# Optimization experiments

Measured on AMD Instinct MI355X. Metric: run time of the kernel, lower is better.

## Reference

```python
import jax, jax.numpy as jnp
import numpy as np

jax.config.update("jax_enable_x64", True)  # 64-bit hashes for collision-free WL signatures

N_NODES = 100_000
N_FEATURES = 64
N_EDGES = 6_400_000
NUM_ITERATIONS = 3
STEP = 1


def setup_inputs() -> dict:
    key = jax.random.key(0)
    kx, ke = jax.random.split(key)
    x = jax.random.normal(kx, (N_NODES, N_FEATURES), dtype=jnp.float32)  # one-hot-ish label scores
    edge_index = jax.random.randint(ke, (2, N_EDGES), 0, N_NODES, dtype=jnp.int64)
    return {"x": x, "edge_index": edge_index}


def _splitmix64(z):
    # High-quality 64-bit mixer (uint64, wraps mod 2^64).
    z = z + jnp.uint64(0x9E3779B97F4A7C15)
    z = (z ^ (z >> jnp.uint64(30))) * jnp.uint64(0xBF58476D1CE4E5B9)
    z = (z ^ (z >> jnp.uint64(27))) * jnp.uint64(0x94D049BB133111EB)
    return z ^ (z >> jnp.uint64(31))


def _wl_conv(colors, src, dst, offset):
    """One WL refinement: hash (own color, multiset of neighbor colors), then
    relabel signatures by first-occurrence order (matches PyG WLConv's dict
    insertion order), continuing the global color counter `offset` (matches the
    persistent hashmap across iterations)."""
    n = colors.shape[0]
    h = _splitmix64(colors.astype(jnp.uint64) + jnp.uint64(1))
    # multiset of neighbor colors -> order-invariant sum of neighbor hashes
    nb_sum = jnp.zeros(n, dtype=jnp.uint64).at[dst].add(h[src])  # [N]
    sig = _splitmix64(h * jnp.uint64(0x100000001B3) + nb_sum)    # [N] signatures
    # first-occurrence relabeling (stable, deterministic)
    _, inv = jnp.unique(sig, size=n, fill_value=jnp.uint64(0), return_inverse=True)
    idx = jnp.arange(n, dtype=jnp.int64)
    first_idx = jax.ops.segment_min(idx, inv, num_segments=n)  # empty segments -> int64 max
    order = jnp.argsort(first_idx)                              # real uniques come first
    ranks = jnp.zeros(n, dtype=jnp.int64).at[order].set(idx)
    new_colors = offset + ranks[inv]
    num_new = jnp.sum(first_idx < n).astype(jnp.int64)
    return new_colors, offset + num_new


def reference(x, edge_index):
    src, dst = edge_index[0], edge_index[1]
    colors = jnp.argmax(x, axis=1).astype(jnp.int64)  # [N]
    feats = [colors]
    offset = jnp.int64(0)
    for _ in range(NUM_ITERATIONS):
        for _ in range(STEP):
            colors, offset = _wl_conv(colors, src, dst, offset)
        feats.append(colors)
    return jnp.stack(feats, axis=-1)  # [N, NUM_ITERATIONS+1], int64
```

## Files before the change

### kernel.cpp

```cpp
#include <hip/hip_runtime.h>

typedef unsigned long long u64;
typedef unsigned int u32;
typedef unsigned char u8;
typedef int  v4i __attribute__((ext_vector_type(4)));
typedef unsigned int v4u __attribute__((ext_vector_type(4)));

#define TBL_BITS 18
#define TBL_SIZE (1u << TBL_BITS)
#define TBL_MASK (TBL_SIZE - 1u)
#define EMPTY_KEY 0xFFFFFFFFFFFFFFFFull

#define BK_BITS 9
#define BK_SZ   512
#define MAXNB   256
#define PBLK    2048
#define LDSE    3200
#define NSUB    8
#define GSTR    16

__device__ __forceinline__ u64 splitmix64(u64 z) {
    z = z + 0x9E3779B97F4A7C15ull;
    z = (z ^ (z >> 30)) * 0xBF58476D1CE4E5B9ull;
    z = (z ^ (z >> 27)) * 0x94D049BB133111EBull;
    return z ^ (z >> 31);
}

__device__ __forceinline__ v4i nt_load4(const int* p) {
    return __builtin_nontemporal_load((const v4i*)p);
}
__device__ __forceinline__ v4u nt_loadu4(const u32* p) {
    return __builtin_nontemporal_load((const v4u*)p);
}

__global__ __launch_bounds__(256) void partition_argmax(const float* __restrict__ x,
                                                        const int* __restrict__ src,
                                                        const int* __restrict__ dst,
                                                        u32* __restrict__ gcur,
                                                        u32* __restrict__ packed,
                                                        u64* __restrict__ h,
                                                        int* __restrict__ out,
                                                        int n, int mI4, int nbuck, int cap, int per) {
    int t = threadIdx.x, b = blockIdx.x;
    {
        int wv = (b * 256 + t) >> 6, lane = t & 63;
        const int WPG = (PBLK * 256) >> 6;
        for (int row = wv; row < n; row += WPG) {
            float v = x[(size_t)row * 64 + lane];
            int idx = lane;
            #pragma unroll
            for (int off = 32; off >= 1; off >>= 1) {
                float ov = __shfl_xor(v, off);
                int   oi = __shfl_xor(idx, off);
                if (ov > v || (ov == v && oi < idx)) { v = ov; idx = oi; }
            }
            if (lane == 0) {
                h[row] = splitmix64((u64)idx + 1ull);
                out[(size_t)row * 4 + 0] = idx;
            }
        }
    }
    __shared__ u32 pk[LDSE];
    __shared__ u32 spk[LDSE];
    __shared__ u8  bd[LDSE];
    __shared__ u8  sbd[LDSE];
    __shared__ u32 hist[256], adjB[256], cur[256];
    __shared__ u32 wsum[4];
    hist[t] = 0u;
    __syncthreads();
    int i0 = b * per;
    int i1 = i0 + per; if (i1 > mI4) i1 = mI4;
    int nI = i1 - i0; if (nI < 0) nI = 0;
    int nE = nI * 4;
    for (int i = t; i < nI; i += 256) {
        v4i dv = nt_load4(dst + 4 * (size_t)(i0 + i));
        v4i sv = nt_load4(src + 4 * (size_t)(i0 + i));
        u32 d, s, bid;
        d = (u32)dv.x; s = (u32)sv.x; bid = d >> BK_BITS;
        pk[4*i+0] = (s << BK_BITS) | (d & (BK_SZ-1u)); bd[4*i+0] = (u8)bid; atomicAdd(&hist[bid], 1u);
        d = (u32)dv.y; s = (u32)sv.y; bid = d >> BK_BITS;
        pk[4*i+1] = (s << BK_BITS) | (d & (BK_SZ-1u)); bd[4*i+1] = (u8)bid; atomicAdd(&hist[bid], 1u);
        d = (u32)dv.z; s = (u32)sv.z; bid = d >> BK_BITS;
        pk[4*i+2] = (s << BK_BITS) | (d & (BK_SZ-1u)); bd[4*i+2] = (u8)bid; atomicAdd(&hist[bid], 1u);
        d = (u32)dv.w; s = (u32)sv.w; bid = d >> BK_BITS;
        pk[4*i+3] = (s << BK_BITS) | (d & (BK_SZ-1u)); bd[4*i+3] = (u8)bid; atomicAdd(&hist[bid], 1u);
    }
    __syncthreads();
    u32 v = hist[t];
    int lane = t & 63, w = t >> 6;
    int x2 = (int)v;
    #pragma unroll
    for (int o = 1; o < 64; o <<= 1) {
        int y = __shfl_up(x2, o);
        if (lane >= o) x2 += y;
    }
    if (lane == 63) wsum[w] = (u32)x2;
    __syncthreads();
    u32 woff = 0;
    for (int ww = 0; ww < w; ++ww) woff += wsum[ww];
    u32 excl = woff + (u32)x2 - v;
    cur[t] = excl;
    if (t < nbuck && v > 0u) {
        u32 bpos = atomicAdd(&gcur[t * GSTR], v);
        if (bpos > (u32)cap - v) bpos = (u32)cap - v;
        adjB[t] = (u32)t * (u32)cap + bpos - excl;
    }
    __syncthreads();
    for (int i = t; i < nE; i += 256) {
        u32 bb = (u32)bd[i];
        u32 p = atomicAdd(&cur[bb], 1u);
        spk[p] = pk[i];
        sbd[p] = (u8)bb;
    }
    __syncthreads();
    for (int p = t; p < nE; p += 256) {
        packed[adjB[sbd[p]] + (u32)p] = spk[p];
    }
}

__global__ __launch_bounds__(256) void nb_kernel(const u32* __restrict__ packed,
                                                 const u32* __restrict__ gcur,
                                                 const u64* __restrict__ h,
                                                 u64* __restrict__ nb8, size_t nstride,
                                                 u64* __restrict__ keys,
                                                 u32* __restrict__ vals, int nbuck, int cap) {
    int b = blockIdx.x, t = threadIdx.x;
    if (b >= nbuck * NSUB) {
        int base = (b - nbuck * NSUB) * 1024;
        for (int k = t; k < 1024; k += 256) { keys[base + k] = EMPTY_KEY; vals[base + k] = 0xFFFFFFFFu; }
        return;
    }
    int bucket = b >> 3, sub = b & 7;
    __shared__ u64 acc[BK_SZ];
    acc[t] = 0ull; acc[t + 256] = 0ull;
    __syncthreads();
    u32 lo = (u32)bucket * (u32)cap;
    u32 len = gcur[bucket * GSTR];
    u32 q0 = ((len * (u32)sub) >> 3) & ~3u;
    u32 q1 = (sub == 7) ? len : (((len * (u32)(sub + 1)) >> 3) & ~3u);
    u32 nv4 = (q1 - q0) >> 2;
    const u32* pbase = packed + lo + q0;
    for (u32 i = (u32)t; i < nv4; i += 256) {
        v4u vv = nt_loadu4(pbase + 4 * (size_t)i);
        atomicAdd(&acc[vv.x & (BK_SZ - 1u)], h[vv.x >> BK_BITS]);
        atomicAdd(&acc[vv.y & (BK_SZ - 1u)], h[vv.y >> BK_BITS]);
        atomicAdd(&acc[vv.z & (BK_SZ - 1u)], h[vv.z >> BK_BITS]);
        atomicAdd(&acc[vv.w & (BK_SZ - 1u)], h[vv.w >> BK_BITS]);
    }
    for (u32 e = q0 + nv4 * 4 + (u32)t; e < q1; e += 256) {
        u32 vv = packed[lo + e];
        atomicAdd(&acc[vv & (BK_SZ - 1u)], h[vv >> BK_BITS]);
    }
    __syncthreads();
    u64* dstp = nb8 + (size_t)sub * nstride + ((size_t)bucket << BK_BITS);
    dstp[t] = acc[t];
    dstp[t + 256] = acc[t + 256];
}

__global__ void sig_kernel8(const u64* __restrict__ h, const u64* __restrict__ nb8,
                            size_t nstride, u32* __restrict__ slotarr,
                            u64* __restrict__ keys, u32* __restrict__ vals, int n) {
    int i = blockIdx.x * blockDim.x + threadIdx.x;
    if (i >= n) return;
    u64 nbv = 0;
    #pragma unroll
    for (int s = 0; s < NSUB; ++s) nbv += nb8[(size_t)s * nstride + i];
    u64 sg = splitmix64(h[i] * 0x100000001B3ull + nbv);
    u32 slot = (u32)sg & TBL_MASK;
    while (true) {
        u64 k = keys[slot];
        if (k == sg) break;
        if (k == EMPTY_KEY) {
            u64 prev = atomicCAS(&keys[slot], (u64)EMPTY_KEY, sg);
            if (prev == EMPTY_KEY || prev == sg) break;
        }
        slot = (slot + 1u) & TBL_MASK;
    }
    atomicMin(&vals[slot], (u32)i);
    slotarr[i] = slot;
}

__global__ void sig_kernel1(const u64* __restrict__ h, const u64* __restrict__ nb,
                            u32* __restrict__ slotarr, u64* __restrict__ keys,
                            u32* __restrict__ vals, int n) {
    int i = blockIdx.x * blockDim.x + threadIdx.x;
    if (i >= n) return;
    u64 sg = splitmix64(h[i] * 0x100000001B3ull + nb[i]);
    u32 slot = (u32)sg & TBL_MASK;
    while (true) {
        u64 k = keys[slot];
        if (k == sg) break;
        if (k == EMPTY_KEY) {
            u64 prev = atomicCAS(&keys[slot], (u64)EMPTY_KEY, sg);
            if (prev == EMPTY_KEY || prev == sg) break;
        }
        slot = (slot + 1u) & TBL_MASK;
    }
    atomicMin(&vals[slot], (u32)i);
    slotarr[i] = slot;
}

__global__ void count_rank(const u32* __restrict__ slotarr, const u32* __restrict__ vals,
                           u32* __restrict__ f, u32* __restrict__ lrank,
                           u32* __restrict__ partials, int n) {
    int b = blockIdx.x, t = threadIdx.x;
    int i = b * 256 + t;
    u32 isf = 0, fi = 0;
    if (i < n) {
        fi = vals[slotarr[i]];
        f[i] = fi;
        isf = (fi == (u32)i) ? 1u : 0u;
    }
    __shared__ u32 wsum[4];
    u32 lane = t & 63, wv = (u32)t >> 6;
    int x = (int)isf;
    #pragma unroll
    for (int o = 1; o < 64; o <<= 1) {
        int y = __shfl_up(x, o);
        if (lane >= (u32)o) x += y;
    }
    if (lane == 63) wsum[wv] = (u32)x;
    __syncthreads();
    u32 woff = 0;
    for (u32 w = 0; w < wv; ++w) woff += wsum[w];
    if (i < n) lrank[i] = woff + (u32)x - isf;
    if (t == 255) partials[b] = woff + (u32)x;
}

__global__ __launch_bounds__(512) void relabel_fused(const u32* __restrict__ f,
                                                     const u32* __restrict__ lrank,
                                                     const u32* __restrict__ partials,
                                                     u32* __restrict__ offsets, int iter,
                                                     u64* __restrict__ h, int* __restrict__ out,
                                                     int n, int npb) {
    __shared__ u32 pp[512];
    __shared__ u32 ws[8];
    int t = threadIdx.x;
    u32 v = (t < npb) ? partials[t] : 0u;
    int lane = t & 63, w = t >> 6;
    int x = (int)v;
    #pragma unroll
    for (int o = 1; o < 64; o <<= 1) {
        int y = __shfl_up(x, o);
        if (lane >= o) x += y;
    }
    if (lane == 63) ws[w] = (u32)x;
    __syncthreads();
    u32 woff = 0;
    for (int ww = 0; ww < w; ++ww) woff += ws[ww];
    u32 incl = woff + (u32)x;
    pp[t] = incl - v;
    if (blockIdx.x == 0 && t == 511) offsets[iter + 1] = offsets[iter] + incl;
    __syncthreads();
    int i = blockIdx.x * 512 + t;
    if (i >= n) return;
    u32 j = f[i];
    u32 c = offsets[iter] + pp[j >> 8] + lrank[j];
    h[i] = splitmix64((u64)c + 1ull);
    out[(size_t)i * 4 + (iter + 1)] = (int)c;
}


__global__ void argmax_kernel(const float* __restrict__ x, u64* __restrict__ h,
                              int* __restrict__ out, u32* __restrict__ offsets, int n) {
    if (blockIdx.x == 0 && threadIdx.x == 0) offsets[0] = 0u;
    int wave = (int)((blockIdx.x * (u32)blockDim.x + threadIdx.x) >> 6);
    int lane = threadIdx.x & 63;
    if (wave >= n) return;
    float v = x[(size_t)wave * 64 + lane];
    int idx = lane;
    #pragma unroll
    for (int off = 32; off >= 1; off >>= 1) {
        float ov = __shfl_xor(v, off);
        int   oi = __shfl_xor(idx, off);
        if (ov > v || (ov == v && oi < idx)) { v = ov; idx = oi; }
    }
    if (lane == 0) {
        h[wave] = splitmix64((u64)idx + 1ull);
        out[(size_t)wave * 4 + 0] = idx;
    }
}

__global__ void init_iter_kernel(u64* __restrict__ keys, u32* __restrict__ vals,
                                 u64* __restrict__ nb, int n) {
    int i = blockIdx.x * blockDim.x + threadIdx.x;
    if (i < (int)TBL_SIZE) { keys[i] = EMPTY_KEY; vals[i] = 0xFFFFFFFFu; }
    if (i < n) nb[i] = 0ull;
}

__global__ void edge_kernel(const int* __restrict__ src, const int* __restrict__ dst,
                            const u64* __restrict__ h, u64* __restrict__ nb, int m) {
    int stride = gridDim.x * blockDim.x;
    for (int e = blockIdx.x * blockDim.x + threadIdx.x; e < m; e += stride) {
        atomicAdd(&nb[(u32)dst[e]], h[(u32)src[e]]);
    }
}

extern "C" void kernel_launch(void* const* d_in, const int* in_sizes, int n_in,
                              void* d_out, int out_size, void* d_ws, size_t ws_size,
                              hipStream_t stream) {
    const float* x = (const float*)d_in[0];
    const int* ei = (const int*)d_in[1];
    int n = in_sizes[0] / 64;
    int m = in_sizes[1] / 2;
    const int* src = ei;
    const int* dst = ei + m;
    int* out = (int*)d_out;

    const int NPB = (n + 255) / 256;
    const int NRB = (n + 511) / 512;
    const int nbuck = (n + BK_SZ - 1) >> BK_BITS;
    const size_t nstride = (size_t)nbuck << BK_BITS;
    const int mI4 = m >> 2;
    const int per = (mI4 + PBLK - 1) / PBLK;
    const int cap = (int)((((size_t)m / (size_t)(nbuck > 0 ? nbuck : 1)) * 9 / 8 + 2048 + 255) & ~(size_t)255);

    auto align = [](size_t v) { return (v + 255) & ~(size_t)255; };
    const size_t meta_bytes = ((size_t)(MAXNB * GSTR) + 16) * 4;
    size_t sz_meta   = align(meta_bytes);
    size_t sz_packed = align((size_t)nbuck * (size_t)cap * 4);
    size_t sz_h      = align((size_t)n * 8);
    size_t sz_nbp    = align(nstride * 8 * NSUB);
    size_t sz_tblk   = align((size_t)TBL_SIZE * 8);
    size_t sz_tblv   = align((size_t)TBL_SIZE * 4);
    size_t sz_n4     = align((size_t)n * 4);
    size_t sz_small  = align((size_t)512 * 4);
    size_t need_fast = sz_meta + sz_packed + sz_h + sz_nbp + sz_tblk + sz_tblv
                     + 3 * sz_n4 + sz_small + 256;

    char* p = (char*)d_ws;
    bool fast = (ws_size >= need_fast) && (nbuck <= MAXNB) && ((m & 3) == 0)
              && (NPB <= 512) && (per * 4 <= LDSE) && (n >= 256);
    if (fast) {
        u32* meta    = (u32*)p; p += sz_meta;
        u32* gcur    = meta;
        u32* offsets = meta + MAXNB * GSTR;
        u32* packed  = (u32*)p; p += sz_packed;
        u64* h       = (u64*)p; p += sz_h;
        u64* nbp     = (u64*)p; p += sz_nbp;
        u64* keys    = (u64*)p; p += sz_tblk;
        u32* vals    = (u32*)p; p += sz_tblv;
        u32* slotarr = (u32*)p; p += sz_n4;
        u32* f       = (u32*)p; p += sz_n4;
        u32* lrank   = (u32*)p; p += sz_n4;
        u32* partials= (u32*)p;

        hipMemsetAsync(d_ws, 0, meta_bytes, stream);
        partition_argmax<<<PBLK, 256, 0, stream>>>(x, src, dst, gcur, packed, h, out,
                                                   n, mI4, nbuck, cap, per);
        for (int it = 0; it < 3; ++it) {
            nb_kernel    <<<nbuck * NSUB + 256, 256, 0, stream>>>(packed, gcur, h,
                                                                  nbp, nstride, keys, vals, nbuck, cap);
            sig_kernel8  <<<NPB, 256, 0, stream>>>(h, nbp, nstride, slotarr, keys, vals, n);
            count_rank   <<<NPB, 256, 0, stream>>>(slotarr, vals, f, lrank, partials, n);
            relabel_fused<<<NRB, 512, 0, stream>>>(f, lrank, partials, offsets, it, h, out, n, NPB);
        }
    } else {
        u64* h       = (u64*)p; p += sz_h;
        u64* nb      = (u64*)p; p += sz_h;
        u64* keys    = (u64*)p; p += sz_tblk;
        u32* vals    = (u32*)p; p += sz_tblv;
        u32* slotarr = (u32*)p; p += sz_n4;
        u32* f       = (u32*)p; p += sz_n4;
        u32* lrank   = (u32*)p; p += sz_n4;
        u32* partials= (u32*)p; p += sz_small;
        u32* offsets = (u32*)p;

        argmax_kernel<<<(n + 3) / 4, 256, 0, stream>>>(x, h, out, offsets, n);
        for (int it = 0; it < 3; ++it) {
            init_iter_kernel<<<(TBL_SIZE + 255) / 256, 256, 0, stream>>>(keys, vals, nb, n);
            edge_kernel  <<<4096, 256, 0, stream>>>(src, dst, h, nb, m);
            sig_kernel1  <<<NPB, 256, 0, stream>>>(h, nb, slotarr, keys, vals, n);
            count_rank   <<<NPB, 256, 0, stream>>>(slotarr, vals, f, lrank, partials, n);
            relabel_fused<<<NRB, 512, 0, stream>>>(f, lrank, partials, offsets, it, h, out, n, NPB);
        }
    }
}
```

Measured before the change: 266.1 us.

## Split argmax from partition, halve nb sub-splits, separate partial scan from relabel

Three changes are bundled. The argmax is moved out of the fused partition kernel into its own one-wave-per-row launch. The per-bucket neighbor accumulation now uses 4 sub-blocks instead of 8, so the signature kernel sums four partial arrays instead of eight. The fused relabel kernel, where every block redundantly scanned the block partials, is replaced by a single-block scan kernel plus a 256-thread relabel kernel. This cuts redundant scan work and partial-sum traffic, but adds kernel launches per iteration and gives less parallelism in nb_kernel.

```diff
diff --git a/kernel.cpp b/kernel.cpp
--- a/kernel.cpp
+++ b/kernel.cpp
@@ -16,7 +16,7 @@
 #define MAXNB   256
 #define PBLK    2048
 #define LDSE    3200
-#define NSUB    8
+#define NSUB    4
 #define GSTR    16
 
 __device__ __forceinline__ u64 splitmix64(u64 z) {
@@ -33,39 +33,38 @@
     return __builtin_nontemporal_load((const v4u*)p);
 }
 
-__global__ __launch_bounds__(256) void partition_argmax(const float* __restrict__ x,
-                                                        const int* __restrict__ src,
+__global__ void argmax_kernel(const float* __restrict__ x, u64* __restrict__ h,
+                              int* __restrict__ out, u32* __restrict__ offsets, int n) {
+    if (blockIdx.x == 0 && threadIdx.x == 0) offsets[0] = 0u;
+    int wave = (int)((blockIdx.x * (u32)blockDim.x + threadIdx.x) >> 6);
+    int lane = threadIdx.x & 63;
+    if (wave >= n) return;
+    float v = x[(size_t)wave * 64 + lane];
+    int idx = lane;
+    #pragma unroll
+    for (int off = 32; off >= 1; off >>= 1) {
+        float ov = __shfl_xor(v, off);
+        int   oi = __shfl_xor(idx, off);
+        if (ov > v || (ov == v && oi < idx)) { v = ov; idx = oi; }
+    }
+    if (lane == 0) {
+        h[wave] = splitmix64((u64)idx + 1ull);
+        out[(size_t)wave * 4 + 0] = idx;
+    }
+}
+
+__global__ __launch_bounds__(256) void partition_kernel(const int* __restrict__ src,
                                                         const int* __restrict__ dst,
                                                         u32* __restrict__ gcur,
                                                         u32* __restrict__ packed,
-                                                        u64* __restrict__ h,
-                                                        int* __restrict__ out,
-                                                        int n, int mI4, int nbuck, int cap, int per) {
-    int t = threadIdx.x, b = blockIdx.x;
-    {
-        int wv = (b * 256 + t) >> 6, lane = t & 63;
-        const int WPG = (PBLK * 256) >> 6;
-        for (int row = wv; row < n; row += WPG) {
-            float v = x[(size_t)row * 64 + lane];
-            int idx = lane;
-            #pragma unroll
-            for (int off = 32; off >= 1; off >>= 1) {
-                float ov = __shfl_xor(v, off);
-                int   oi = __shfl_xor(idx, off);
-                if (ov > v || (ov == v && oi < idx)) { v = ov; idx = oi; }
-            }
-            if (lane == 0) {
-                h[row] = splitmix64((u64)idx + 1ull);
-                out[(size_t)row * 4 + 0] = idx;
-            }
-        }
-    }
+                                                        int mI4, int nbuck, int cap, int per) {
     __shared__ u32 pk[LDSE];
     __shared__ u32 spk[LDSE];
     __shared__ u8  bd[LDSE];
     __shared__ u8  sbd[LDSE];
     __shared__ u32 hist[256], adjB[256], cur[256];
     __shared__ u32 wsum[4];
+    int t = threadIdx.x, b = blockIdx.x;
     hist[t] = 0u;
     __syncthreads();
     int i0 = b * per;
@@ -121,7 +120,7 @@
 __global__ __launch_bounds__(256) void nb_kernel(const u32* __restrict__ packed,
                                                  const u32* __restrict__ gcur,
                                                  const u64* __restrict__ h,
-                                                 u64* __restrict__ nb8, size_t nstride,
+                                                 u64* __restrict__ nbp, size_t nstride,
                                                  u64* __restrict__ keys,
                                                  u32* __restrict__ vals, int nbuck, int cap) {
     int b = blockIdx.x, t = threadIdx.x;
@@ -130,14 +129,14 @@
         for (int k = t; k < 1024; k += 256) { keys[base + k] = EMPTY_KEY; vals[base + k] = 0xFFFFFFFFu; }
         return;
     }
-    int bucket = b >> 3, sub = b & 7;
+    int bucket = b >> 2, sub = b & 3;
     __shared__ u64 acc[BK_SZ];
     acc[t] = 0ull; acc[t + 256] = 0ull;
     __syncthreads();
     u32 lo = (u32)bucket * (u32)cap;
     u32 len = gcur[bucket * GSTR];
-    u32 q0 = ((len * (u32)sub) >> 3) & ~3u;
-    u32 q1 = (sub == 7) ? len : (((len * (u32)(sub + 1)) >> 3) & ~3u);
+    u32 q0 = ((len * (u32)sub) >> 2) & ~3u;
+    u32 q1 = (sub == NSUB - 1) ? len : (((len * (u32)(sub + 1)) >> 2) & ~3u);
     u32 nv4 = (q1 - q0) >> 2;
     const u32* pbase = packed + lo + q0;
     for (u32 i = (u32)t; i < nv4; i += 256) {
@@ -152,19 +151,17 @@
         atomicAdd(&acc[vv & (BK_SZ - 1u)], h[vv >> BK_BITS]);
     }
     __syncthreads();
-    u64* dstp = nb8 + (size_t)sub * nstride + ((size_t)bucket << BK_BITS);
+    u64* dstp = nbp + (size_t)sub * nstride + ((size_t)bucket << BK_BITS);
     dstp[t] = acc[t];
     dstp[t + 256] = acc[t + 256];
 }
 
-__global__ void sig_kernel8(const u64* __restrict__ h, const u64* __restrict__ nb8,
+__global__ void sig_kernel4(const u64* __restrict__ h, const u64* __restrict__ nbp,
                             size_t nstride, u32* __restrict__ slotarr,
                             u64* __restrict__ keys, u32* __restrict__ vals, int n) {
     int i = blockIdx.x * blockDim.x + threadIdx.x;
     if (i >= n) return;
-    u64 nbv = 0;
-    #pragma unroll
-    for (int s = 0; s < NSUB; ++s) nbv += nb8[(size_t)s * nstride + i];
+    u64 nbv = nbp[i] + nbp[nstride + i] + nbp[2 * nstride + i] + nbp[3 * nstride + i];
     u64 sg = splitmix64(h[i] * 0x100000001B3ull + nbv);
     u32 slot = (u32)sg & TBL_MASK;
     while (true) {
@@ -178,6 +175,76 @@
     }
     atomicMin(&vals[slot], (u32)i);
     slotarr[i] = slot;
+}
+
+__global__ void count_rank(const u32* __restrict__ slotarr, const u32* __restrict__ vals,
+                           u32* __restrict__ f, u32* __restrict__ lrank,
+                           u32* __restrict__ partials, int n) {
+    int b = blockIdx.x, t = threadIdx.x;
+    int i = b * 256 + t;
+    u32 isf = 0, fi = 0;
+    if (i < n) {
+        fi = vals[slotarr[i]];
+        f[i] = fi;
+        isf = (fi == (u32)i) ? 1u : 0u;
+    }
+    __shared__ u32 wsum[4];
+    u32 lane = t & 63, wv = (u32)t >> 6;
+    int x = (int)isf;
+    #pragma unroll
+    for (int o = 1; o < 64; o <<= 1) {
+        int y = __shfl_up(x, o);
+        if (lane >= (u32)o) x += y;
+    }
+    if (lane == 63) wsum[wv] = (u32)x;
+    __syncthreads();
+    u32 woff = 0;
+    for (u32 w = 0; w < wv; ++w) woff += wsum[w];
+    if (i < n) lrank[i] = woff + (u32)x - isf;
+    if (t == 255) partials[b] = woff + (u32)x;
+}
+
+__global__ void scan_partials(const u32* __restrict__ partials, u32* __restrict__ pp,
+                              u32* __restrict__ offsets, int iter, int nblk) {
+    __shared__ u32 A[512], B[512];
+    int t = threadIdx.x;
+    u32 v = (t < nblk) ? partials[t] : 0u;
+    A[t] = v; __syncthreads();
+    u32 *cur = A, *nxt = B;
+    for (int o = 1; o < 512; o <<= 1) {
+        u32 y = cur[t] + ((t >= o) ? cur[t - o] : 0u);
+        nxt[t] = y; __syncthreads();
+        u32* tmp = cur; cur = nxt; nxt = tmp;
+    }
+    if (t < nblk) pp[t] = cur[t] - v;
+    if (t == 511) offsets[iter + 1] = offsets[iter] + cur[511];
+}
+
+__global__ void relabel_fast(const u32* __restrict__ f, const u32* __restrict__ lrank,
+                             const u32* __restrict__ pp, const u32* __restrict__ offsets,
+                             int iter, u64* __restrict__ h, int* __restrict__ out, int n) {
+    int i = blockIdx.x * 256 + threadIdx.x;
+    if (i >= n) return;
+    u32 j = f[i];
+    u32 c = offsets[iter] + pp[j >> 8] + lrank[j];
+    h[i] = splitmix64((u64)c + 1ull);
+    out[(size_t)i * 4 + (iter + 1)] = (int)c;
+}
+
+
+__global__ void init_iter_kernel(u64* __restrict__ keys, u32* __restrict__ vals,
+                                 u64* __restrict__ nb, int n) {
+    int i = blockIdx.x * blockDim.x + threadIdx.x;
+    if (i < (int)TBL_SIZE) { keys[i] = EMPTY_KEY; vals[i] = 0xFFFFFFFFu; }
+    if (i < n) nb[i] = 0ull;
+}
+
+__global__ void edge_kernel(const int* __restrict__ src, const int* __restrict__ dst,
+                            const u64* __restrict__ h, u64* __restrict__ nb, int m) {
+    int stride = gridDim.x * blockDim.x;
+    for (int e = blockIdx.x * blockDim.x + threadIdx.x; e < m; e += stride) {
+        atomicAdd(&nb[(u32)dst[e]], h[(u32)src[e]]);
+    }
 }
 
 __global__ void sig_kernel1(const u64* __restrict__ h, const u64* __restrict__ nb,
@@ -200,102 +267,6 @@
     slotarr[i] = slot;
 }
 
-__global__ void count_rank(const u32* __restrict__ slotarr, const u32* __restrict__ vals,
-                           u32* __restrict__ f, u32* __restrict__ lrank,
-                           u32* __restrict__ partials, int n) {
-    int b = blockIdx.x, t = threadIdx.x;
-    int i = b * 256 + t;
-    u32 isf = 0, fi = 0;
-    if (i < n) {
-        fi = vals[slotarr[i]];
-        f[i] = fi;
-        isf = (fi == (u32)i) ? 1u : 0u;
-    }
-    __shared__ u32 wsum[4];
-    u32 lane = t & 63, wv = (u32)t >> 6;
-    int x = (int)isf;
-    #pragma unroll
-    for (int o = 1; o < 64; o <<= 1) {
-        int y = __shfl_up(x, o);
-        if (lane >= (u32)o) x += y;
-    }
-    if (lane == 63) wsum[wv] = (u32)x;
-    __syncthreads();
-    u32 woff = 0;
-    for (u32 w = 0; w < wv; ++w) woff += wsum[w];
-    if (i < n) lrank[i] = woff + (u32)x - isf;
-    if (t == 255) partials[b] = woff + (u32)x;
-}
-
-__global__ __launch_bounds__(512) void relabel_fused(const u32* __restrict__ f,
-                                                     const u32* __restrict__ lrank,
-                                                     const u32* __restrict__ partials,
-                                                     u32* __restrict__ offsets, int iter,
-                                                     u64* __restrict__ h, int* __restrict__ out,
-                                                     int n, int npb) {
-    __shared__ u32 pp[512];
-    __shared__ u32 ws[8];
-    int t = threadIdx.x;
-    u32 v = (t < npb) ? partials[t] : 0u;
-    int lane = t & 63, w = t >> 6;
-    int x = (int)v;
-    #pragma unroll
-    for (int o = 1; o < 64; o <<= 1) {
-        int y = __shfl_up(x, o);
-        if (lane >= o) x += y;
-    }
-    if (lane == 63) ws[w] = (u32)x;
-    __syncthreads();
-    u32 woff = 0;
-    for (int ww = 0; ww < w; ++ww) woff += ws[ww];
-    u32 incl = woff + (u32)x;
-    pp[t] = incl - v;
-    if (blockIdx.x == 0 && t == 511) offsets[iter + 1] = offsets[iter] + incl;
-    __syncthreads();
-    int i = blockIdx.x * 512 + t;
-    if (i >= n) return;
-    u32 j = f[i];
-    u32 c = offsets[iter] + pp[j >> 8] + lrank[j];
-    h[i] = splitmix64((u64)c + 1ull);
-    out[(size_t)i * 4 + (iter + 1)] = (int)c;
-}
-
-
-__global__ void argmax_kernel(const float* __restrict__ x, u64* __restrict__ h,
-                              int* __restrict__ out, u32* __restrict__ offsets, int n) {
-    if (blockIdx.x == 0 && threadIdx.x == 0) offsets[0] = 0u;
-    int wave = (int)((blockIdx.x * (u32)blockDim.x + threadIdx.x) >> 6);
-    int lane = threadIdx.x & 63;
-    if (wave >= n) return;
-    float v = x[(size_t)wave * 64 + lane];
-    int idx = lane;
-    #pragma unroll
-    for (int off = 32; off >= 1; off >>= 1) {
-        float ov = __shfl_xor(v, off);
-        int   oi = __shfl_xor(idx, off);
-        if (ov > v || (ov == v && oi < idx)) { v = ov; idx = oi; }
-    }
-    if (lane == 0) {
-        h[wave] = splitmix64((u64)idx + 1ull);
-        out[(size_t)wave * 4 + 0] = idx;
-    }
-}
-
-__global__ void init_iter_kernel(u64* __restrict__ keys, u32* __restrict__ vals,
-                                 u64* __restrict__ nb, int n) {
-    int i = blockIdx.x * blockDim.x + threadIdx.x;
-    if (i < (int)TBL_SIZE) { keys[i] = EMPTY_KEY; vals[i] = 0xFFFFFFFFu; }
-    if (i < n) nb[i] = 0ull;
-}
-
-__global__ void edge_kernel(const int* __restrict__ src, const int* __restrict__ dst,
-                            const u64* __restrict__ h, u64* __restrict__ nb, int m) {
-    int stride = gridDim.x * blockDim.x;
-    for (int e = blockIdx.x * blockDim.x + threadIdx.x; e < m; e += stride) {
-        atomicAdd(&nb[(u32)dst[e]], h[(u32)src[e]]);
-    }
-}
-
 extern "C" void kernel_launch(void* const* d_in, const int* in_sizes, int n_in,
                               void* d_out, int out_size, void* d_ws, size_t ws_size,
                               hipStream_t stream) {
@@ -308,7 +279,6 @@
     int* out = (int*)d_out;
 
     const int NPB = (n + 255) / 256;
-    const int NRB = (n + 511) / 512;
     const int nbuck = (n + BK_SZ - 1) >> BK_BITS;
     const size_t nstride = (size_t)nbuck << BK_BITS;
     const int mI4 = m >> 2;
@@ -326,7 +296,7 @@
     size_t sz_n4     = align((size_t)n * 4);
     size_t sz_small  = align((size_t)512 * 4);
     size_t need_fast = sz_meta + sz_packed + sz_h + sz_nbp + sz_tblk + sz_tblv
-                     + 3 * sz_n4 + sz_small + 256;
+                     + 3 * sz_n4 + 2 * sz_small + 256;
 
     char* p = (char*)d_ws;
     bool fast = (ws_size >= need_fast) && (nbuck <= MAXNB) && ((m & 3) == 0)
@@ -343,17 +313,20 @@
         u32* slotarr = (u32*)p; p += sz_n4;
         u32* f       = (u32*)p; p += sz_n4;
         u32* lrank   = (u32*)p; p += sz_n4;
-        u32* partials= (u32*)p;
+        u32* partials= (u32*)p; p += sz_small;
+        u32* pp      = (u32*)p;
 
         hipMemsetAsync(d_ws, 0, meta_bytes, stream);
-        partition_argmax<<<PBLK, 256, 0, stream>>>(x, src, dst, gcur, packed, h, out,
-                                                   n, mI4, nbuck, cap, per);
+        argmax_kernel<<<(n + 3) / 4, 256, 0, stream>>>(x, h, out, offsets, n);
+        partition_kernel<<<PBLK, 256, 0, stream>>>(src, dst, gcur, packed, mI4, nbuck, cap, per);
+
         for (int it = 0; it < 3; ++it) {
             nb_kernel    <<<nbuck * NSUB + 256, 256, 0, stream>>>(packed, gcur, h,
                                                                   nbp, nstride, keys, vals, nbuck, cap);
-            sig_kernel8  <<<NPB, 256, 0, stream>>>(h, nbp, nstride, slotarr, keys, vals, n);
+            sig_kernel4  <<<NPB, 256, 0, stream>>>(h, nbp, nstride, slotarr, keys, vals, n);
             count_rank   <<<NPB, 256, 0, stream>>>(slotarr, vals, f, lrank, partials, n);
-            relabel_fused<<<NRB, 512, 0, stream>>>(f, lrank, partials, offsets, it, h, out, n, NPB);
+            scan_partials<<<1, 512, 0, stream>>>(partials, pp, offsets, it, NPB);
+            relabel_fast <<<NPB, 256, 0, stream>>>(f, lrank, pp, offsets, it, h, out, n);
         }
     } else {
         u64* h       = (u64*)p; p += sz_h;
@@ -364,6 +337,7 @@
         u32* f       = (u32*)p; p += sz_n4;
         u32* lrank   = (u32*)p; p += sz_n4;
         u32* partials= (u32*)p; p += sz_small;
+        u32* pp      = (u32*)p; p += sz_small;
         u32* offsets = (u32*)p;
 
         argmax_kernel<<<(n + 3) / 4, 256, 0, stream>>>(x, h, out, offsets, n);
@@ -372,7 +346,8 @@
             edge_kernel  <<<4096, 256, 0, stream>>>(src, dst, h, nb, m);
             sig_kernel1  <<<NPB, 256, 0, stream>>>(h, nb, slotarr, keys, vals, n);
             count_rank   <<<NPB, 256, 0, stream>>>(slotarr, vals, f, lrank, partials, n);
-            relabel_fused<<<NRB, 512, 0, stream>>>(f, lrank, partials, offsets, it, h, out, n, NPB);
+            scan_partials<<<1, 512, 0, stream>>>(partials, pp, offsets, it, NPB);
+            relabel_fast <<<NPB, 256, 0, stream>>>(f, lrank, pp, offsets, it, h, out, n);
         }
     }
 }
```

New measurement: 268.2 us. Within noise of the previous version (+0.8%).
